# Optimization experiments

Measured on AMD Instinct MI355X. Metric: run time of the kernel, lower is better.

## Reference

```python
import jax, jax.numpy as jnp
import numpy as np

N, F, K, E = 50000, 128, 8, 1600000


def setup_inputs() -> dict:
    key = jax.random.key(0)
    k1, k2, k3, k4 = jax.random.split(key, 4)
    x = jax.random.normal(k1, (N, F), dtype=jnp.float32)
    adj = jax.random.randint(k2, (2, E), 0, N, dtype=jnp.int64)
    e = jax.random.normal(k3, (N, K), dtype=jnp.float32)
    stdv = 1.0 / np.sqrt(F)  # reset_parameters: uniform(-stdv, stdv)
    weights = jax.random.uniform(k4, (K, 2 * F, F), dtype=jnp.float32,
                                 minval=-stdv, maxval=stdv)
    return {"x": x, "adj": adj, "e": e, "weights": weights}


def _gcn_conv(x, row, col, n_nodes):
    # degree of each node as a message *destination* (col) -- matches torch degree(col, N)
    deg = jax.ops.segment_sum(jnp.ones(row.shape[0], x.dtype), col,
                              num_segments=n_nodes)
    val = (1.0 / jnp.sqrt(deg[col])) * (1.0 / jnp.sqrt(deg[row]))
    val = jnp.nan_to_num(val, nan=0.0, posinf=0.0, neginf=0.0)
    # SparseTensor(row=col, col=row) @ x : aggregate x[row] into col
    msg = val[:, None] * x[row]           # [E, F] gather
    return jax.ops.segment_sum(msg, col, num_segments=n_nodes)  # [N, F] scatter


def reference(x, adj, e, weights):
    n_nodes = x.shape[0]
    row, col = adj[0], adj[1]
    hi = _gcn_conv(x, row, col, n_nodes)                  # [N, F]
    hi = jnp.concatenate([hi, x], axis=1)                 # [N, 2F]
    # torch: repeat hi K times, bmm with [K,2F,F], transpose -> [N, K, F]
    outputs = jnp.einsum('nf,kfo->nko', hi, weights)      # [N, K, F]
    out = jnp.sum(e[:, :, None] * outputs, axis=1)        # gating sum over K
    out = out + x                                         # residual
    return out
```

## Files before the change

### kernel.cpp

```cpp
#include <hip/hip_runtime.h>
#include <hip/hip_bf16.h>

typedef __bf16 bf16_t;
typedef __bf16 bf16x8 __attribute__((ext_vector_type(8)));
typedef float f32x4 __attribute__((ext_vector_type(4)));
typedef float f32x2 __attribute__((ext_vector_type(2)));

#define F 128
#define KEXP 8
#define BM 256
#define BSTG 32768

#define NB 196
#define CAP 12288
#define CH 8192

__global__ __launch_bounds__(256) void k_binA(const int* __restrict__ row,
    const int* __restrict__ col, int* __restrict__ cursor,
    int* __restrict__ region, int E){
  __shared__ int stage[CH];
  __shared__ unsigned char stageb[CH];
  __shared__ int hist4[4][NB];
  __shared__ int lcur4[4][NB];
  int tid = threadIdx.x, wid = tid >> 6;
  int base = blockIdx.x * CH;
  int cnt = min(CH, E - base);
  for (int i = tid; i < 4*NB; i += 256) ((int*)hist4)[i] = 0;
  __syncthreads();
  for (int i = tid; i < cnt; i += 256){
    int r = row[base+i], c = col[base+i];
    stage[i] = (r << 8) | (c & 255);
    stageb[i] = (unsigned char)(c >> 8);
    atomicAdd(&hist4[wid][c >> 8], 1);
  }
  __syncthreads();
  for (int b = tid; b < NB; b += 256){
    int h0 = hist4[0][b], h1 = hist4[1][b], h2 = hist4[2][b], h3 = hist4[3][b];
    int gbase = atomicAdd(&cursor[b], h0+h1+h2+h3) + b*CAP;
    lcur4[0][b] = gbase;
    lcur4[1][b] = gbase + h0;
    lcur4[2][b] = gbase + h0 + h1;
    lcur4[3][b] = gbase + h0 + h1 + h2;
  }
  __syncthreads();
  for (int i = tid; i < cnt; i += 256){
    int b = stageb[i];
    int pos = atomicAdd(&lcur4[wid][b], 1);
    region[pos] = stage[i];
  }
}

__global__ void k_bstart(const int* __restrict__ cursor, int* __restrict__ bstart,
                         int* __restrict__ offs, int Nn){
  __shared__ int lds[256];
  int t = threadIdx.x;
  int c = (t < NB) ? cursor[t] : 0;
  lds[t] = c; __syncthreads();
  for (int off=1; off<256; off<<=1){
    int u = (t>=off) ? lds[t-off] : 0;
    __syncthreads();
    lds[t] += u;
    __syncthreads();
  }
  if (t < NB) bstart[t] = lds[t] - c;
  if (t == NB-1){ bstart[NB] = lds[t]; offs[Nn] = lds[t]; }
}

__global__ __launch_bounds__(256) void k_binB(const int* __restrict__ region,
    const int* __restrict__ cursor, const int* __restrict__ bstart,
    int* __restrict__ deg, int* __restrict__ offs, int* __restrict__ bucket,
    int Nn){
  __shared__ int hist4[4][256];
  __shared__ int loff[256];
  __shared__ int lcur4[4][256];
  int b = blockIdx.x, t = threadIdx.x, wid = t >> 6;
  int cnt = cursor[b];
  const int* src = region + b*CAP;
  for (int i = t; i < 4*256; i += 256) ((int*)hist4)[i] = 0;
  __syncthreads();
  for (int i = t; i < cnt; i += 256) atomicAdd(&hist4[wid][src[i] & 255], 1);
  __syncthreads();
  int h0 = hist4[0][t], h1 = hist4[1][t], h2 = hist4[2][t], h3 = hist4[3][t];
  int v = h0 + h1 + h2 + h3;
  loff[t] = v;
  __syncthreads();
  for (int off=1; off<256; off<<=1){
    int u = (t>=off) ? loff[t-off] : 0;
    __syncthreads();
    loff[t] += u;
    __syncthreads();
  }
  int excl = loff[t] - v;
  int gb = bstart[b];
  int node = b*256 + t;
  if (node < Nn){ deg[node] = v; offs[node] = gb + excl; }
  lcur4[0][t] = gb + excl;
  lcur4[1][t] = gb + excl + h0;
  lcur4[2][t] = gb + excl + h0 + h1;
  lcur4[3][t] = gb + excl + h0 + h1 + h2;
  __syncthreads();
  for (int i = t; i < cnt; i += 256){
    int p = src[i];
    int pos = atomicAdd(&lcur4[wid][p & 255], 1);
    bucket[pos] = p >> 8;
  }
}

__global__ void k_prep(const float* __restrict__ x, const int* __restrict__ deg,
                       unsigned int* __restrict__ xs8, const float* __restrict__ W,
                       bf16_t* __restrict__ Wt, int Nn, int xsB){
  int tid = threadIdx.x;
  if ((int)blockIdx.x < xsB){
    int i = blockIdx.x*256 + tid;
    if (i < Nn*16){
      int n = i >> 4;
      int d = deg[n];
      float dr = d>0 ? rsqrtf((float)d) : 0.f;
      const float4 f0 = *reinterpret_cast<const float4*>(&x[(size_t)i*8]);
      const float4 f1 = *reinterpret_cast<const float4*>(&x[(size_t)i*8+4]);
      unsigned int lo, hi2;
      lo  = __builtin_amdgcn_cvt_pk_fp8_f32(dr*f0.x, dr*f0.y, 0,  false);
      lo  = __builtin_amdgcn_cvt_pk_fp8_f32(dr*f0.z, dr*f0.w, lo, true);
      hi2 = __builtin_amdgcn_cvt_pk_fp8_f32(dr*f1.x, dr*f1.y, 0,  false);
      hi2 = __builtin_amdgcn_cvt_pk_fp8_f32(dr*f1.z, dr*f1.w, hi2, true);
      xs8[(size_t)i*2]     = lo;
      xs8[(size_t)i*2 + 1] = hi2;
    }
  } else {
    int i8 = (blockIdx.x - xsB)*256 + tid;
    if (i8 < 32768){
      int kk   = i8 >> 12;
      int frag = (i8 >> 6) & 63;
      int lane = i8 & 63;
      int ks = frag >> 3, cg = frag & 7;
      int n  = cg*16 + (lane & 15);
      int f0 = ks*32 + (lane >> 4)*8;
      bf16x8 v;
      #pragma unroll
      for (int j=0;j<8;j++)
        v[j] = (bf16_t)W[(size_t)kk*32768 + (size_t)(f0+j)*128 + n];
      *reinterpret_cast<bf16x8*>(&Wt[(size_t)i8*8]) = v;
    }
  }
}

__global__ __launch_bounds__(256) void k_agg(const unsigned int* __restrict__ xs8,
    const int* __restrict__ offs, const int* __restrict__ bucket,
    bf16_t* __restrict__ hi, int Nn){
  int wid = threadIdx.x >> 6, lane = threadIdx.x & 63;
  int g = lane >> 4, j16 = lane & 15;
  int n = blockIdx.x*16 + wid*4 + g;
  if (n >= Nn) return;
  int o0 = offs[n], o1 = offs[n+1];
  float acc[8] = {0.f,0.f,0.f,0.f,0.f,0.f,0.f,0.f};
  int nr = (o1 - o0 + 7) >> 3;
  int j = o0;
  for (int r = 0; r < nr; r++, j += 8){
    int idx[8];
    #pragma unroll
    for (int t=0;t<8;t++) idx[t] = bucket[min(j+t, o1-1)];
    uint2 v[8];
    #pragma unroll
    for (int t=0;t<8;t++)
      v[t] = *reinterpret_cast<const uint2*>(
          reinterpret_cast<const unsigned char*>(xs8) + (size_t)idx[t]*F + j16*8);
    #pragma unroll
    for (int t=0;t<8;t++){
      float m = (j+t < o1) ? 1.f : 0.f;
      f32x2 p0 = __builtin_amdgcn_cvt_pk_f32_fp8(v[t].x, false);
      f32x2 p1 = __builtin_amdgcn_cvt_pk_f32_fp8(v[t].x, true);
      f32x2 p2 = __builtin_amdgcn_cvt_pk_f32_fp8(v[t].y, false);
      f32x2 p3 = __builtin_amdgcn_cvt_pk_f32_fp8(v[t].y, true);
      acc[0] += m*p0.x; acc[1] += m*p0.y;
      acc[2] += m*p1.x; acc[3] += m*p1.y;
      acc[4] += m*p2.x; acc[5] += m*p2.y;
      acc[6] += m*p3.x; acc[7] += m*p3.y;
    }
  }
  int dn = o1 - o0;
  float dc = dn>0 ? rsqrtf((float)dn) : 0.f;
  bf16x8 o;
  #pragma unroll
  for (int i=0;i<8;i++) o[i] = (bf16_t)(dc*acc[i]);
  *reinterpret_cast<bf16x8*>(&hi[(size_t)n*F + j16*8]) = o;
}

#define MFMA_BF16 __builtin_amdgcn_mfma_f32_16x16x32_bf16

__global__ __launch_bounds__(512, 2) void k_gemm(
    const bf16_t* __restrict__ hi, const float* __restrict__ x,
    const float* __restrict__ e, const bf16_t* __restrict__ Wt,
    float* __restrict__ out, int Nn)
{
  extern __shared__ __align__(16) char smem[];
  bf16_t* b_s  = (bf16_t*)smem;
  float*  e_sT = (float*)(smem + 2*BSTG*2);
  const int tid = threadIdx.x;
  const int base = blockIdx.x * BM;
  const int lane = tid & 63, wid = tid >> 6;
  const int rw = wid >> 1, cw = wid & 1;
  const int r16 = lane & 15, kc = lane >> 4;

  #pragma unroll
  for (int i=0;i<8;i++){
    int u = tid + i*512;
    __builtin_amdgcn_global_load_lds(
        (const __attribute__((address_space(1))) void*)(Wt + (size_t)u*8),
        (__attribute__((address_space(3))) void*)(b_s + (size_t)u*8),
        16, 0, 0);
  }

  for (int i = tid; i < KEXP*BM; i += 512){
    int kk = i >> 8, row = i & (BM-1);
    int srow = min(base + row, Nn-1);
    e_sT[kk*BM + row] = e[(size_t)srow*KEXP + kk];
  }

  int rr[4];
  #pragma unroll
  for (int rg=0; rg<4; rg++) rr[rg] = min(base + rw*64 + rg*16 + r16, Nn-1);
  bf16x8 a[4][8];
  #pragma unroll
  for (int rg=0; rg<4; rg++){
    #pragma unroll
    for (int ks=0; ks<4; ks++)
      a[rg][ks] = *reinterpret_cast<const bf16x8*>(
          &hi[(size_t)rr[rg]*F + ks*32 + kc*8]);
    #pragma unroll
    for (int ks=0; ks<4; ks++){
      const float4 f0 = *reinterpret_cast<const float4*>(
          &x[(size_t)rr[rg]*F + ks*32 + kc*8]);
      const float4 f1 = *reinterpret_cast<const float4*>(
          &x[(size_t)rr[rg]*F + ks*32 + kc*8 + 4]);
      bf16x8 v;
      v[0]=(bf16_t)f0.x; v[1]=(bf16_t)f0.y; v[2]=(bf16_t)f0.z; v[3]=(bf16_t)f0.w;
      v[4]=(bf16_t)f1.x; v[5]=(bf16_t)f1.y; v[6]=(bf16_t)f1.z; v[7]=(bf16_t)f1.w;
      a[rg][4+ks] = v;
    }
  }

  f32x4 acc[4][4];
  #pragma unroll
  for (int rg=0;rg<4;rg++)
    #pragma unroll
    for (int cg=0;cg<4;cg++) acc[rg][cg] = (f32x4){0.f,0.f,0.f,0.f};
  const f32x4 fz = (f32x4){0.f,0.f,0.f,0.f};

  asm volatile("s_waitcnt vmcnt(0) lgkmcnt(0)" ::: "memory");
  __builtin_amdgcn_s_barrier();

  for (int kk=0; kk<8; kk++){
    if (kk < 7){
      const bf16_t* src = Wt + (size_t)(kk+1)*BSTG;
      bf16_t* dst = b_s + ((kk+1)&1)*BSTG;
      #pragma unroll
      for (int i=0;i<8;i++){
        int u = tid + i*512;
        __builtin_amdgcn_global_load_lds(
            (const __attribute__((address_space(1))) void*)(src + (size_t)u*8),
            (__attribute__((address_space(3))) void*)(dst + (size_t)u*8),
            16, 0, 0);
      }
      asm volatile("s_waitcnt vmcnt(8)" ::: "memory");
    } else {
      asm volatile("s_waitcnt vmcnt(0)" ::: "memory");
    }
    __builtin_amdgcn_s_barrier();

    const bf16_t* buf = b_s + (kk&1)*BSTG;
    f32x4 ev[4];
    #pragma unroll
    for (int rg=0; rg<4; rg++)
      ev[rg] = *reinterpret_cast<const f32x4*>(
          &e_sT[kk*BM + rw*64 + rg*16 + kc*4]);

    __builtin_amdgcn_s_setprio(1);
    #pragma unroll
    for (int cg=0; cg<4; cg++){
      f32x4 ck[4];
      {
        bf16x8 b = *reinterpret_cast<const bf16x8*>(
            &buf[(size_t)(cw*4 + cg)*512 + lane*8]);
        #pragma unroll
        for (int rg=0; rg<4; rg++)
          ck[rg] = MFMA_BF16(a[rg][0], b, fz, 0, 0, 0);
      }
      #pragma unroll
      for (int ks=1; ks<8; ks++){
        bf16x8 b = *reinterpret_cast<const bf16x8*>(
            &buf[(size_t)(ks*8 + cw*4 + cg)*512 + lane*8]);
        #pragma unroll
        for (int rg=0; rg<4; rg++)
          ck[rg] = MFMA_BF16(a[rg][ks], b, ck[rg], 0, 0, 0);
      }
      #pragma unroll
      for (int rg=0; rg<4; rg++)
        #pragma unroll
        for (int r=0; r<4; r++)
          acc[rg][cg][r] += ev[rg][r]*ck[rg][r];
    }
    __builtin_amdgcn_s_setprio(0);

    __builtin_amdgcn_s_barrier();
  }

  #pragma unroll
  for (int rg=0; rg<4; rg++){
    #pragma unroll
    for (int cg=0; cg<4; cg++){
      int ocol = cw*64 + cg*16 + r16;
      #pragma unroll
      for (int r=0; r<4; r++){
        int node = base + rw*64 + rg*16 + kc*4 + r;
        if (node < Nn)
          out[(size_t)node*F + ocol] = acc[rg][cg][r] + x[(size_t)node*F + ocol];
      }
    }
  }
}

extern "C" void kernel_launch(void* const* d_in, const int* in_sizes, int n_in,
                              void* d_out, int out_size, void* d_ws, size_t ws_size,
                              hipStream_t stream){
  const float* x  = (const float*)d_in[0];
  const int*  adj = (const int*)d_in[1];
  const float* e  = (const float*)d_in[2];
  const float* W  = (const float*)d_in[3];
  float* out = (float*)d_out;
  int Nn = in_sizes[0] / F;
  int E  = in_sizes[1] / 2;
  const int* rowp = adj;
  const int* colp = adj + E;

  char* w = (char*)d_ws;
  auto alloc = [&](size_t b){ char* p = w; w += (b + 255) & ~(size_t)255; return p; };
  int* deg     = (int*)alloc((size_t)Nn*4);
  int* offs    = (int*)alloc(((size_t)Nn+1)*4);
  int* cursor  = (int*)alloc((size_t)NB*4);
  int* bstart  = (int*)alloc((size_t)(NB+1)*4);
  int* bucket  = (int*)alloc((size_t)E*4);
  char* uni    = alloc((size_t)NB*CAP*4);
  int* region  = (int*)uni;
  unsigned int* xs8 = (unsigned int*)uni;
  bf16_t* hi   = (bf16_t*)alloc((size_t)Nn*F*2);
  bf16_t* Wt   = (bf16_t*)alloc((size_t)2048*F*2);

  const int smem_bytes = 2*BSTG*2 + KEXP*BM*4;
  hipFuncSetAttribute((const void*)k_gemm,
                      hipFuncAttributeMaxDynamicSharedMemorySize, smem_bytes);

  int nchunks = (E + CH - 1) / CH;
  int xsB = (Nn*16 + 255)/256;
  hipMemsetAsync(cursor, 0, (size_t)NB*4, stream);
  k_binA<<<nchunks, 256, 0, stream>>>(rowp, colp, cursor, region, E);
  k_bstart<<<1, 256, 0, stream>>>(cursor, bstart, offs, Nn);
  k_binB<<<NB, 256, 0, stream>>>(region, cursor, bstart, deg, offs, bucket, Nn);
  k_prep<<<xsB + 128, 256, 0, stream>>>(x, deg, xs8, W, Wt, Nn, xsB);
  k_agg<<<(Nn+15)/16, 256, 0, stream>>>(xs8, offs, bucket, hi, Nn);
  k_gemm<<<(Nn+BM-1)/BM, 512, smem_bytes, stream>>>(hi, x, e, Wt, out, Nn);
}
```

Before: 142.7 us.

## Split GEMM into half-column blocks with smaller row tiles and single-buffered weights

The gated GEMM now uses 128-row tiles and splits output columns across two blocks. Each 256-thread block loads only its half of each expert's weight slice (32 KB) into static LDS, and the weight layout in k_prep is reordered to match. The goal is many more blocks (about 782 instead of 196) and lower register and LDS use per block, so occupancy and CU coverage improve. In exchange, double buffering is dropped: every expert step waits for its weight load before computing, and each A row and the x conversion are loaded twice, once per column half.

```diff
diff --git a/kernel.cpp b/kernel.cpp
--- a/kernel.cpp
+++ b/kernel.cpp
@@ -8,8 +8,8 @@
 
 #define F 128
 #define KEXP 8
-#define BM 256
-#define BSTG 32768
+#define BMG 128
+#define NSTG 16384
 
 #define NB 196
 #define CAP 12288
@@ -129,11 +129,13 @@
   } else {
     int i8 = (blockIdx.x - xsB)*256 + tid;
     if (i8 < 32768){
-      int kk   = i8 >> 12;
-      int frag = (i8 >> 6) & 63;
-      int lane = i8 & 63;
-      int ks = frag >> 3, cg = frag & 7;
-      int n  = cg*16 + (lane & 15);
+      int st   = i8 >> 11;
+      int g    = i8 & 2047;
+      int frag = g >> 6;
+      int lane = g & 63;
+      int kk = st >> 1, nh = st & 1;
+      int ks = frag >> 2, cg = frag & 3;
+      int n  = nh*64 + cg*16 + (lane & 15);
       int f0 = ks*32 + (lane >> 4)*8;
       bf16x8 v;
       #pragma unroll
@@ -187,41 +189,31 @@
 
 #define MFMA_BF16 __builtin_amdgcn_mfma_f32_16x16x32_bf16
 
-__global__ __launch_bounds__(512, 2) void k_gemm(
+__global__ __launch_bounds__(256, 3) void k_gemm(
     const bf16_t* __restrict__ hi, const float* __restrict__ x,
     const float* __restrict__ e, const bf16_t* __restrict__ Wt,
     float* __restrict__ out, int Nn)
 {
-  extern __shared__ __align__(16) char smem[];
-  bf16_t* b_s  = (bf16_t*)smem;
-  float*  e_sT = (float*)(smem + 2*BSTG*2);
+  __shared__ alignas(16) bf16_t b_s[NSTG];
+  __shared__ float e_sT[KEXP*BMG];
   const int tid = threadIdx.x;
-  const int base = blockIdx.x * BM;
-  const int lane = tid & 63, wid = tid >> 6;
-  const int rw = wid >> 1, cw = wid & 1;
+  const int rblk = blockIdx.x >> 1, nh = blockIdx.x & 1;
+  const int base = rblk * BMG;
+  const int lane = tid & 63, rw = tid >> 6;
   const int r16 = lane & 15, kc = lane >> 4;
 
+  for (int i = tid; i < KEXP*BMG; i += 256){
+    int kk = i >> 7, row = i & (BMG-1);
+    int srow = min(base + row, Nn-1);
+    e_sT[kk*BMG + row] = e[(size_t)srow*KEXP + kk];
+  }
+
+  int rr[2];
+  rr[0] = min(base + rw*32 + r16,      Nn-1);
+  rr[1] = min(base + rw*32 + 16 + r16, Nn-1);
+  bf16x8 a[2][8];
   #pragma unroll
-  for (int i=0;i<8;i++){
-    int u = tid + i*512;
-    __builtin_amdgcn_global_load_lds(
-        (const __attribute__((address_space(1))) void*)(Wt + (size_t)u*8),
-        (__attribute__((address_space(3))) void*)(b_s + (size_t)u*8),
-        16, 0, 0);
-  }
-
-  for (int i = tid; i < KEXP*BM; i += 512){
-    int kk = i >> 8, row = i & (BM-1);
-    int srow = min(base + row, Nn-1);
-    e_sT[kk*BM + row] = e[(size_t)srow*KEXP + kk];
-  }
-
-  int rr[4];
-  #pragma unroll
-  for (int rg=0; rg<4; rg++) rr[rg] = min(base + rw*64 + rg*16 + r16, Nn-1);
-  bf16x8 a[4][8];
-  #pragma unroll
-  for (int rg=0; rg<4; rg++){
+  for (int rg=0; rg<2; rg++){
     #pragma unroll
     for (int ks=0; ks<4; ks++)
       a[rg][ks] = *reinterpret_cast<const bf16x8*>(
@@ -239,62 +231,50 @@
     }
   }
 
-  f32x4 acc[4][4];
+  f32x4 acc[2][4];
   #pragma unroll
-  for (int rg=0;rg<4;rg++)
+  for (int rg=0;rg<2;rg++)
     #pragma unroll
     for (int cg=0;cg<4;cg++) acc[rg][cg] = (f32x4){0.f,0.f,0.f,0.f};
   const f32x4 fz = (f32x4){0.f,0.f,0.f,0.f};
 
-  asm volatile("s_waitcnt vmcnt(0) lgkmcnt(0)" ::: "memory");
-  __builtin_amdgcn_s_barrier();
+  const bf16_t* wbase = Wt + (size_t)nh*NSTG;
 
   for (int kk=0; kk<8; kk++){
-    if (kk < 7){
-      const bf16_t* src = Wt + (size_t)(kk+1)*BSTG;
-      bf16_t* dst = b_s + ((kk+1)&1)*BSTG;
-      #pragma unroll
-      for (int i=0;i<8;i++){
-        int u = tid + i*512;
-        __builtin_amdgcn_global_load_lds(
-            (const __attribute__((address_space(1))) void*)(src + (size_t)u*8),
-            (__attribute__((address_space(3))) void*)(dst + (size_t)u*8),
-            16, 0, 0);
-      }
-      asm volatile("s_waitcnt vmcnt(8)" ::: "memory");
-    } else {
-      asm volatile("s_waitcnt vmcnt(0)" ::: "memory");
-    }
+    const bf16_t* src = wbase + (size_t)kk*2*NSTG;
+    #pragma unroll
+    for (int i=0;i<8;i++){
+      int u = tid + i*256;
+      __builtin_amdgcn_global_load_lds(
+          (const __attribute__((address_space(1))) void*)(src + (size_t)u*8),
+          (__attribute__((address_space(3))) void*)(b_s + (size_t)u*8),
+          16, 0, 0);
+    }
+    asm volatile("s_waitcnt vmcnt(0) lgkmcnt(0)" ::: "memory");
     __builtin_amdgcn_s_barrier();
 
-    const bf16_t* buf = b_s + (kk&1)*BSTG;
-    f32x4 ev[4];
-    #pragma unroll
-    for (int rg=0; rg<4; rg++)
-      ev[rg] = *reinterpret_cast<const f32x4*>(
-          &e_sT[kk*BM + rw*64 + rg*16 + kc*4]);
+    f32x4 ev[2];
+    ev[0] = *reinterpret_cast<const f32x4*>(&e_sT[kk*BMG + rw*32 + kc*4]);
+    ev[1] = *reinterpret_cast<const f32x4*>(&e_sT[kk*BMG + rw*32 + 16 + kc*4]);
 
     __builtin_amdgcn_s_setprio(1);
     #pragma unroll
     for (int cg=0; cg<4; cg++){
-      f32x4 ck[4];
+      f32x4 ck[2];
       {
-        bf16x8 b = *reinterpret_cast<const bf16x8*>(
-            &buf[(size_t)(cw*4 + cg)*512 + lane*8]);
-        #pragma unroll
-        for (int rg=0; rg<4; rg++)
-          ck[rg] = MFMA_BF16(a[rg][0], b, fz, 0, 0, 0);
+        bf16x8 b = *reinterpret_cast<const bf16x8*>(&b_s[(size_t)cg*512 + lane*8]);
+        ck[0] = MFMA_BF16(a[0][0], b, fz, 0, 0, 0);
+        ck[1] = MFMA_BF16(a[1][0], b, fz, 0, 0, 0);
       }
       #pragma unroll
       for (int ks=1; ks<8; ks++){
         bf16x8 b = *reinterpret_cast<const bf16x8*>(
-            &buf[(size_t)(ks*8 + cw*4 + cg)*512 + lane*8]);
-        #pragma unroll
-        for (int rg=0; rg<4; rg++)
-          ck[rg] = MFMA_BF16(a[rg][ks], b, ck[rg], 0, 0, 0);
+            &b_s[(size_t)(ks*4 + cg)*512 + lane*8]);
+        ck[0] = MFMA_BF16(a[0][ks], b, ck[0], 0, 0, 0);
+        ck[1] = MFMA_BF16(a[1][ks], b, ck[1], 0, 0, 0);
       }
       #pragma unroll
-      for (int rg=0; rg<4; rg++)
+      for (int rg=0; rg<2; rg++)
         #pragma unroll
         for (int r=0; r<4; r++)
           acc[rg][cg][r] += ev[rg][r]*ck[rg][r];
@@ -305,13 +285,13 @@
   }
 
   #pragma unroll
-  for (int rg=0; rg<4; rg++){
+  for (int rg=0; rg<2; rg++){
     #pragma unroll
     for (int cg=0; cg<4; cg++){
-      int ocol = cw*64 + cg*16 + r16;
+      int ocol = nh*64 + cg*16 + r16;
       #pragma unroll
       for (int r=0; r<4; r++){
-        int node = base + rw*64 + rg*16 + kc*4 + r;
+        int node = base + rw*32 + rg*16 + kc*4 + r;
         if (node < Nn)
           out[(size_t)node*F + ocol] = acc[rg][cg][r] + x[(size_t)node*F + ocol];
       }
@@ -345,17 +325,14 @@
   bf16_t* hi   = (bf16_t*)alloc((size_t)Nn*F*2);
   bf16_t* Wt   = (bf16_t*)alloc((size_t)2048*F*2);
 
-  const int smem_bytes = 2*BSTG*2 + KEXP*BM*4;
-  hipFuncSetAttribute((const void*)k_gemm,
-                      hipFuncAttributeMaxDynamicSharedMemorySize, smem_bytes);
-
   int nchunks = (E + CH - 1) / CH;
   int xsB = (Nn*16 + 255)/256;
+  int gblk = ((Nn + BMG - 1)/BMG) * 2;
   hipMemsetAsync(cursor, 0, (size_t)NB*4, stream);
   k_binA<<<nchunks, 256, 0, stream>>>(rowp, colp, cursor, region, E);
   k_bstart<<<1, 256, 0, stream>>>(cursor, bstart, offs, Nn);
   k_binB<<<NB, 256, 0, stream>>>(region, cursor, bstart, deg, offs, bucket, Nn);
   k_prep<<<xsB + 128, 256, 0, stream>>>(x, deg, xs8, W, Wt, Nn, xsB);
   k_agg<<<(Nn+15)/16, 256, 0, stream>>>(xs8, offs, bucket, hi, Nn);
-  k_gemm<<<(Nn+BM-1)/BM, 512, smem_bytes, stream>>>(hi, x, e, Wt, out, Nn);
-}
+  k_gemm<<<gblk, 256, 0, stream>>>(hi, x, e, Wt, out, Nn);
+}
```

After: 264.3 us. +85.2%, slower.
